# Optimization experiments

Hardware: AMD Instinct MI355X
Metric: run time of the kernel (lower is better)

The kernel has to match this reference:

```python
import jax, jax.numpy as jnp
import numpy as np

B, T, Y, H = 1024, 13, 188, 512  # batch, window, feature dim, GRU hidden
DECODE_STEPS = 13


def setup_inputs() -> dict:
    key = jax.random.key(0)
    ks = jax.random.split(key, 12)
    s = 1.0 / np.sqrt(H)  # torch GRU/Linear default init scale
    u = lambda k, shape: jax.random.uniform(k, shape, jnp.float32, -s, s)
    return {
        "x": jax.random.normal(ks[0], (B, T, Y), jnp.float32),
        # GRU layer 0 (input_size=Y)
        "W_ih0": u(ks[1], (3 * H, Y)),
        "W_hh0": u(ks[2], (3 * H, H)),
        "b_ih0": u(ks[3], (3 * H,)),
        "b_hh0": u(ks[4], (3 * H,)),
        # GRU layer 1 (input_size=H)
        "W_ih1": u(ks[5], (3 * H, H)),
        "W_hh1": u(ks[6], (3 * H, H)),
        "b_ih1": u(ks[7], (3 * H,)),
        "b_hh1": u(ks[8], (3 * H,)),
        # output Linear H -> Y
        "W_out": u(ks[9], (Y, H)),
        "b_out": u(ks[10], (Y,)),
    }


def _gru_layer(x, W_ih, W_hh, b_ih, b_hh):
    # x: [B, T, D_in]; PyTorch gate order: r, z, n. Fresh zero h0 each call.
    xg = jnp.einsum('btd,gd->btg', x, W_ih) + b_ih      # [B, T, 3H]
    xg = jnp.swapaxes(xg, 0, 1)                          # [T, B, 3H]
    h0 = jnp.zeros((x.shape[0], H), x.dtype)

    def step(h, xg_t):
        gh = h @ W_hh.T + b_hh                           # [B, 3H]
        r = jax.nn.sigmoid(xg_t[:, :H] + gh[:, :H])
        z = jax.nn.sigmoid(xg_t[:, H:2 * H] + gh[:, H:2 * H])
        n = jnp.tanh(xg_t[:, 2 * H:] + r * gh[:, 2 * H:])
        h_new = (1.0 - z) * n + z * h
        return h_new, h_new

    _, hs = jax.lax.scan(step, h0, xg)                   # [T, B, H]
    return jnp.swapaxes(hs, 0, 1)                        # [B, T, H]


def _f(x, W_ih0, W_hh0, b_ih0, b_hh0, W_ih1, W_hh1, b_ih1, b_hh1, W_out, b_out):
    h = _gru_layer(x, W_ih0, W_hh0, b_ih0, b_hh0)
    h = _gru_layer(h, W_ih1, W_hh1, b_ih1, b_hh1)
    h = jax.nn.relu(h)
    return jnp.einsum('bth,yh->bty', h, W_out) + b_out + x  # residual


def reference(x, W_ih0, W_hh0, b_ih0, b_hh0, W_ih1, W_hh1, b_ih1, b_hh1, W_out, b_out):
    params = (W_ih0, W_hh0, b_ih0, b_hh0, W_ih1, W_hh1, b_ih1, b_hh1, W_out, b_out)
    yp = []
    for _ in range(DECODE_STEPS):
        p = _f(x, *params)
        last = p[:, -1:, :]                              # [B, 1, Y]
        yp.append(last[:, 0, :])
        x = jnp.concatenate([x[:, 1:, :], last], axis=1)  # slide window
    return jnp.stack(yp, axis=1)                         # [B, 13, Y]
```

## Files before the change

kernel.cpp:

```cpp
#include <hip/hip_runtime.h>
#include <hip/hip_bf16.h>
#include <math.h>

using bf16 = __hip_bfloat16;

#define BB 1024
#define TT 13
#define YY 188
#define HH 512
#define GG 1536
#define YP 192
#define DS 13
#define NT 96
#define NTO 12

typedef __bf16 bf16x8 __attribute__((ext_vector_type(8)));
typedef float f32x4 __attribute__((ext_vector_type(4)));
typedef float f4 __attribute__((ext_vector_type(4)));

__device__ __forceinline__ float sigf(float x) { return 1.f / (1.f + expf(-x)); }
__device__ __forceinline__ bf16x8 ldf(const bf16* p) {
  return *reinterpret_cast<const bf16x8*>(p);
}
__device__ __forceinline__ f32x4 mf(bf16x8 a, bf16x8 b, f32x4 c) {
  return __builtin_amdgcn_mfma_f32_16x16x32_bf16(a, b, c, 0, 0, 0);
}
__device__ __forceinline__ void split2(float v, bf16& hi, bf16& lo) {
  hi = __float2bfloat16(v);
  lo = __float2bfloat16(v - __bfloat162float(hi));
}

struct GruPhase {
  int ncells;
  int zmask;
  unsigned a1off[13];
  unsigned hoff[13];
  unsigned ooff[13];
};

__global__ void k_swz2(const float* __restrict__ src, bf16* __restrict__ dhi,
                       bf16* __restrict__ dlo, int Nsrc, int Ksrc, int ntiles) {
  int idx = blockIdx.x * 256 + threadIdx.x;
  int l = idx & 63;
  int ktnt = idx >> 6;
  int nt = ktnt % ntiles, kt = ktnt / ntiles;
  int n = nt * 16 + (l & 15);
  int k0 = kt * 32 + (l >> 4) * 8;
#pragma unroll
  for (int j = 0; j < 8; ++j) {
    int k = k0 + j;
    float v = (n < Nsrc && k < Ksrc) ? src[(size_t)n * Ksrc + k] : 0.f;
    bf16 h, lo;
    split2(v, h, lo);
    dhi[(size_t)idx * 8 + j] = h;
    dlo[(size_t)idx * 8 + j] = lo;
  }
}

__global__ void k_setup(const float* __restrict__ x, bf16* __restrict__ th,
                        bf16* __restrict__ tl, float* __restrict__ res) {
  int idx = blockIdx.x * 256 + threadIdx.x;
  const int total = 26 * BB * YP;
  if (idx < total) {
    int k = idx % YP;
    int b = (idx / YP) % BB;
    int s = idx / (YP * BB);
    float v = 0.f;
    if (s < TT && k < YY) v = x[((size_t)b * TT + s) * YY + k];
    bf16 h, lo;
    split2(v, h, lo);
    th[idx] = h; tl[idx] = lo;
  }
  if (idx < BB * YY) {
    int yy = idx % YY;
    int b = idx / YY;
    res[idx] = x[((size_t)b * TT + 12) * YY + yy];
  }
}

template <int KT1>
__global__ __launch_bounds__(256, 2) void gru2(
    const bf16* __restrict__ a1h, const bf16* __restrict__ a1l, int lda1,
    const bf16* __restrict__ W1h, const bf16* __restrict__ W1l,
    const float* __restrict__ b1,
    const bf16* __restrict__ hbh, const bf16* __restrict__ hbl,
    const bf16* __restrict__ W2h, const bf16* __restrict__ W2l,
    const float* __restrict__ b2,
    bf16* __restrict__ obh, bf16* __restrict__ obl,
    GruPhase ph)
{
  __shared__ __align__(16) __bf16 Bl[2][24][512];
  const int tid = threadIdx.x;
  const int w = tid >> 6, l = tid & 63;
  const int lr = l & 15, lq = l >> 4, kq = lq * 8;
  const int cell = blockIdx.y >> 3, rt = blockIdx.y & 7;
  const int cw = blockIdx.x * 64;
  const int m0 = rt * 128 + w * 32;
  const bf16* A1h = a1h + ph.a1off[cell];
  const bf16* A1l = a1l + ph.a1off[cell];
  const bf16* HPh = hbh + ph.hoff[cell];
  const bf16* HPl = hbl + ph.hoff[cell];
  bf16* HOh = obh + ph.ooff[cell];
  bf16* HOl = obl + ph.ooff[cell];
  const int zero_h = (ph.zmask >> cell) & 1;
  const int KT2 = zero_h ? 0 : 16;

  const f32x4 vzero = {0.f, 0.f, 0.f, 0.f};
  f32x4 arz[2][2][4];
  f32x4 axn[2][4], ahn[2][4];
#pragma unroll
  for (int rf = 0; rf < 2; ++rf)
#pragma unroll
    for (int ntl = 0; ntl < 4; ++ntl) {
      arz[rf][0][ntl] = vzero; arz[rf][1][ntl] = vzero;
      axn[rf][ntl] = vzero; ahn[rf][ntl] = vzero;
    }

  int tl2a[6], hlr[6];
  size_t soff[6];
#pragma unroll
  for (int r = 0; r < 6; ++r) {
    const int tl2 = r * 4 + w;
    const int hl = tl2 & 1;
    const int gn = tl2 >> 1;
    const int g = gn >> 2, ntl = gn & 3;
    const int ntg = g * 32 + (cw >> 4) + ntl;
    tl2a[r] = tl2; hlr[r] = hl;
    soff[r] = ((size_t)ntg * 64 + l) * 8;
  }

  auto stage_load = [&](const bf16* Wh, const bf16* Wl2, int ktW,
                        bf16x8 (&v)[6]) {
#pragma unroll
    for (int r = 0; r < 6; ++r)
      v[r] = ldf((hlr[r] ? Wl2 : Wh) + soff[r] + (size_t)ktW * (NT * 512));
  };
  auto stage_write = [&](bf16x8 (&v)[6], int buf) {
#pragma unroll
    for (int r = 0; r < 6; ++r)
      *(bf16x8*)(&Bl[buf][tl2a[r]][l * 8]) = v[r];
  };
  auto aload = [&](const bf16* Ah, const bf16* Al, int lda, int ktA,
                   bf16x8 (&d)[2][2]) {
#pragma unroll
    for (int rf = 0; rf < 2; ++rf) {
      const size_t ao = (size_t)(m0 + rf * 16 + lr) * lda + ktA * 32 + kq;
      d[rf][0] = ldf(Ah + ao);
      d[rf][1] = ldf(Al + ao);
    }
  };
  auto compute = [&](bf16x8 (&a)[2][2], int buf, f32x4 (&an)[2][4]) {
#pragma unroll
    for (int g = 0; g < 3; ++g)
#pragma unroll
      for (int ntl = 0; ntl < 4; ++ntl) {
        int tl2 = (g * 4 + ntl) * 2;
        bf16x8 bh  = *(const bf16x8*)(&Bl[buf][tl2][l * 8]);
        bf16x8 blo = *(const bf16x8*)(&Bl[buf][tl2 + 1][l * 8]);
#pragma unroll
        for (int rf = 0; rf < 2; ++rf) {
          if (g < 2)
            arz[rf][g][ntl] = mf(a[rf][0], blo, mf(a[rf][1], bh,
                                 mf(a[rf][0], bh, arz[rf][g][ntl])));
          else
            an[rf][ntl] = mf(a[rf][0], blo, mf(a[rf][1], bh,
                             mf(a[rf][0], bh, an[rf][ntl])));
        }
      }
  };
  auto acopy = [&](bf16x8 (&dst)[2][2], bf16x8 (&src)[2][2]) {
#pragma unroll
    for (int rf = 0; rf < 2; ++rf) {
      dst[rf][0] = src[rf][0];
      dst[rf][1] = src[rf][1];
    }
  };

  bf16x8 w0[6], w1[6], acur[2][2], anx[2][2];

  stage_load(W1h, W1l, 0, w0);
  aload(A1h, A1l, lda1, 0, acur);
  stage_write(w0, 0);
  __syncthreads();

  for (int kt = 0; kt < KT1; ++kt) {
    const int buf = kt & 1;
    const bool more1 = (kt + 1 < KT1);
    const bool next = more1 || (KT2 > 0);
    if (more1)      { stage_load(W1h, W1l, kt + 1, w1); aload(A1h, A1l, lda1, kt + 1, anx); }
    else if (KT2)   { stage_load(W2h, W2l, 0, w1);      aload(HPh, HPl, HH, 0, anx); }
    compute(acur, buf, axn);
    if (next) stage_write(w1, buf ^ 1);
    __syncthreads();
    if (next) acopy(acur, anx);
  }
  if (KT2) {
    for (int kt = 0; kt < 16; ++kt) {
      const int buf = (KT1 + kt) & 1;
      const bool next = (kt + 1 < 16);
      if (next) { stage_load(W2h, W2l, kt + 1, w1); aload(HPh, HPl, HH, kt + 1, anx); }
      compute(acur, buf, ahn);
      if (next) stage_write(w1, buf ^ 1);
      __syncthreads();
      if (next) acopy(acur, anx);
    }
  }

#pragma unroll
  for (int ntl = 0; ntl < 4; ++ntl) {
    const int col = cw + ntl * 16 + lr;
    const float bx0 = b1[col], bx1 = b1[col + HH], bx2 = b1[col + 2 * HH];
    const float bh0 = b2[col], bh1 = b2[col + HH], bh2 = b2[col + 2 * HH];
#pragma unroll
    for (int rf = 0; rf < 2; ++rf)
#pragma unroll
      for (int i = 0; i < 4; ++i) {
        const int row = m0 + rf * 16 + lq * 4 + i;
        const float rr = sigf(arz[rf][0][ntl][i] + bx0 + bh0);
        const float zz = sigf(arz[rf][1][ntl][i] + bx1 + bh1);
        const float nn = tanhf(axn[rf][ntl][i] + bx2 + rr * (ahn[rf][ntl][i] + bh2));
        float hp = 0.f;
        const size_t hidx = (size_t)row * HH + col;
        if (!zero_h)
          hp = __bfloat162float(HPh[hidx]) + __bfloat162float(HPl[hidx]);
        const float hn = (1.f - zz) * nn + zz * hp;
        bf16 sh, sl;
        split2(hn, sh, sl);
        HOh[hidx] = sh;
        HOl[hidx] = sl;
      }
  }
}

template <int KT1>
__global__ __launch_bounds__(256) void gru2n(
    const bf16* __restrict__ a1h, const bf16* __restrict__ a1l, int lda1,
    const bf16* __restrict__ W1h, const bf16* __restrict__ W1l,
    const float* __restrict__ b1,
    const bf16* __restrict__ hbh, const bf16* __restrict__ hbl,
    const bf16* __restrict__ W2h, const bf16* __restrict__ W2l,
    const float* __restrict__ b2,
    bf16* __restrict__ obh, bf16* __restrict__ obl,
    GruPhase ph)
{
  __shared__ __align__(16) __bf16 Bl[2][12][512];
  const int tid = threadIdx.x;
  const int w = tid >> 6, l = tid & 63;
  const int lr = l & 15, lq = l >> 4, kq = lq * 8;
  const int cell = blockIdx.y >> 3, rt = blockIdx.y & 7;
  const int cw = blockIdx.x * 32;
  const int m0 = rt * 128 + w * 32;
  const bf16* A1h = a1h + ph.a1off[cell];
  const bf16* A1l = a1l + ph.a1off[cell];
  const bf16* HPh = hbh + ph.hoff[cell];
  const bf16* HPl = hbl + ph.hoff[cell];
  bf16* HOh = obh + ph.ooff[cell];
  bf16* HOl = obl + ph.ooff[cell];
  const int zero_h = (ph.zmask >> cell) & 1;
  const int KT2 = zero_h ? 0 : 16;

  const f32x4 vzero = {0.f, 0.f, 0.f, 0.f};
  f32x4 arz[2][2][2];
  f32x4 axn[2][2], ahn[2][2];
#pragma unroll
  for (int rf = 0; rf < 2; ++rf)
#pragma unroll
    for (int ntl = 0; ntl < 2; ++ntl) {
      arz[rf][0][ntl] = vzero; arz[rf][1][ntl] = vzero;
      axn[rf][ntl] = vzero; ahn[rf][ntl] = vzero;
    }

  int tl2a[3], uia[3], hlr[3];
  size_t soff[3];
#pragma unroll
  for (int r = 0; r < 3; ++r) {
    int u = r * 256 + tid;
    int tl2 = u >> 6;
    int ui = u & 63;
    int hl = tl2 & 1;
    int gn = tl2 >> 1;
    int g = gn >> 1, ntl = gn & 1;
    int ntg = g * 32 + (cw >> 4) + ntl;
    tl2a[r] = tl2; uia[r] = ui; hlr[r] = hl;
    soff[r] = ((size_t)ntg * 64 + ui) * 8;
  }

  auto stage_load = [&](const bf16* Wh, const bf16* Wl2, int ktW,
                        bf16x8 (&v)[3]) {
#pragma unroll
    for (int r = 0; r < 3; ++r)
      v[r] = ldf((hlr[r] ? Wl2 : Wh) + soff[r] + (size_t)ktW * (NT * 512));
  };
  auto stage_write = [&](bf16x8 (&v)[3], int buf) {
#pragma unroll
    for (int r = 0; r < 3; ++r)
      *(bf16x8*)(&Bl[buf][tl2a[r]][uia[r] * 8]) = v[r];
  };
  auto aload = [&](const bf16* Ah, const bf16* Al, int lda, int ktA,
                   bf16x8 (&d)[2][2]) {
#pragma unroll
    for (int rf = 0; rf < 2; ++rf) {
      const size_t ao = (size_t)(m0 + rf * 16 + lr) * lda + ktA * 32 + kq;
      d[rf][0] = ldf(Ah + ao);
      d[rf][1] = ldf(Al + ao);
    }
  };
  auto compute = [&](bf16x8 (&a)[2][2], int buf, f32x4 (&an)[2][2]) {
#pragma unroll
    for (int g = 0; g < 3; ++g)
#pragma unroll
      for (int ntl = 0; ntl < 2; ++ntl) {
        int tl2 = (g * 2 + ntl) * 2;
        bf16x8 bh  = *(const bf16x8*)(&Bl[buf][tl2][l * 8]);
        bf16x8 blo = *(const bf16x8*)(&Bl[buf][tl2 + 1][l * 8]);
#pragma unroll
        for (int rf = 0; rf < 2; ++rf) {
          if (g < 2)
            arz[rf][g][ntl] = mf(a[rf][0], blo, mf(a[rf][1], bh,
                                 mf(a[rf][0], bh, arz[rf][g][ntl])));
          else
            an[rf][ntl] = mf(a[rf][0], blo, mf(a[rf][1], bh,
                             mf(a[rf][0], bh, an[rf][ntl])));
        }
      }
  };
  auto acopy = [&](bf16x8 (&dst)[2][2], bf16x8 (&src)[2][2]) {
#pragma unroll
    for (int rf = 0; rf < 2; ++rf) {
      dst[rf][0] = src[rf][0];
      dst[rf][1] = src[rf][1];
    }
  };

  bf16x8 w0[3], w1[3], acur[2][2], anx[2][2];

  stage_load(W1h, W1l, 0, w0);
  aload(A1h, A1l, lda1, 0, acur);
  stage_write(w0, 0);
  __syncthreads();

  for (int kt = 0; kt < KT1; ++kt) {
    const int buf = kt & 1;
    const bool more1 = (kt + 1 < KT1);
    const bool next = more1 || (KT2 > 0);
    if (more1)      { stage_load(W1h, W1l, kt + 1, w1); aload(A1h, A1l, lda1, kt + 1, anx); }
    else if (KT2)   { stage_load(W2h, W2l, 0, w1);      aload(HPh, HPl, HH, 0, anx); }
    compute(acur, buf, axn);
    if (next) stage_write(w1, buf ^ 1);
    __syncthreads();
    if (next) acopy(acur, anx);
  }
  if (KT2) {
    for (int kt = 0; kt < 16; ++kt) {
      const int buf = (KT1 + kt) & 1;
      const bool next = (kt + 1 < 16);
      if (next) { stage_load(W2h, W2l, kt + 1, w1); aload(HPh, HPl, HH, kt + 1, anx); }
      compute(acur, buf, ahn);
      if (next) stage_write(w1, buf ^ 1);
      __syncthreads();
      if (next) acopy(acur, anx);
    }
  }

#pragma unroll
  for (int ntl = 0; ntl < 2; ++ntl) {
    const int col = cw + ntl * 16 + lr;
    const float bx0 = b1[col], bx1 = b1[col + HH], bx2 = b1[col + 2 * HH];
    const float bh0 = b2[col], bh1 = b2[col + HH], bh2 = b2[col + 2 * HH];
#pragma unroll
    for (int rf = 0; rf < 2; ++rf)
#pragma unroll
      for (int i = 0; i < 4; ++i) {
        const int row = m0 + rf * 16 + lq * 4 + i;
        const float rr = sigf(arz[rf][0][ntl][i] + bx0 + bh0);
        const float zz = sigf(arz[rf][1][ntl][i] + bx1 + bh1);
        const float nn = tanhf(axn[rf][ntl][i] + bx2 + rr * (ahn[rf][ntl][i] + bh2));
        float hp = 0.f;
        const size_t hidx = (size_t)row * HH + col;
        if (!zero_h)
          hp = __bfloat162float(HPh[hidx]) + __bfloat162float(HPl[hidx]);
        const float hn = (1.f - zz) * nn + zz * hp;
        bf16 sh, sl;
        split2(hn, sh, sl);
        HOh[hidx] = sh;
        HOl[hidx] = sl;
      }
  }
}

__global__ __launch_bounds__(256) void out_m(
    const bf16* __restrict__ h1h, const bf16* __restrict__ h1l,
    const bf16* __restrict__ Wh, const bf16* __restrict__ Wl,
    const float* __restrict__ bo,
    float* __restrict__ res,
    bf16* __restrict__ yh, bf16* __restrict__ yl,
    float* __restrict__ outp, int d)
{
  const int tid = threadIdx.x;
  const int w = tid >> 6, l = tid & 63;
  const int lr = l & 15, lq = l >> 4, kq = lq * 8;
  const int m0 = blockIdx.y * 128 + w * 32;
  const int cw = blockIdx.x * 64;

  const f32x4 vzero = {0.f, 0.f, 0.f, 0.f};
  f32x4 acc[2][4];
#pragma unroll
  for (int rf = 0; rf < 2; ++rf)
#pragma unroll
    for (int ntl = 0; ntl < 4; ++ntl) acc[rf][ntl] = vzero;

  for (int kt = 0; kt < HH / 32; ++kt) {
    bf16x8 ah[2], al[2];
#pragma unroll
    for (int rf = 0; rf < 2; ++rf) {
      const size_t ao = (size_t)(m0 + rf * 16 + lr) * HH + kt * 32 + kq;
      bf16x8 hh = ldf(h1h + ao);
      bf16x8 hl = ldf(h1l + ao);
#pragma unroll
      for (int j = 0; j < 8; ++j) {
        float v = fmaxf((float)hh[j] + (float)hl[j], 0.f);
        __bf16 vh = (__bf16)v;
        __bf16 vl = (__bf16)(v - (float)vh);
        ah[rf][j] = vh;
        al[rf][j] = vl;
      }
    }
#pragma unroll
    for (int ntl = 0; ntl < 4; ++ntl) {
      const int nt = (cw >> 4) + ntl;
      const size_t bo_ = ((size_t)(kt * NTO + nt) * 64 + l) * 8;
      bf16x8 bh = ldf(Wh + bo_);
      bf16x8 bl = ldf(Wl + bo_);
#pragma unroll
      for (int rf = 0; rf < 2; ++rf)
        acc[rf][ntl] = mf(ah[rf], bl, mf(al[rf], bh,
                          mf(ah[rf], bh, acc[rf][ntl])));
    }
  }

#pragma unroll
  for (int ntl = 0; ntl < 4; ++ntl) {
    const int col = cw + ntl * 16 + lr;
    if (col >= YY) continue;
    const float bc = bo[col];
#pragma unroll
    for (int rf = 0; rf < 2; ++rf)
#pragma unroll
      for (int i = 0; i < 4; ++i) {
        const int row = m0 + rf * 16 + lq * 4 + i;
        const int ridx = row * YY + col;
        float o = acc[rf][ntl][i] + bc + res[ridx];
        res[ridx] = o;
        outp[((size_t)row * DS + d) * YY + col] = o;
        bf16 sh, sl;
        split2(o, sh, sl);
        yh[(size_t)row * YP + col] = sh;
        yl[(size_t)row * YP + col] = sl;
      }
  }
}

extern "C" void kernel_launch(void* const* d_in, const int* in_sizes, int n_in,
                              void* d_out, int out_size, void* d_ws, size_t ws_size,
                              hipStream_t stream)
{
  static const int sig_dict[11] = {2501632, 288768, 786432, 1536, 1536,
                                   786432, 786432, 1536, 1536, 96256, 188};
  int map[11];
  bool dict_ok = (n_in == 11);
  if (dict_ok)
    for (int r = 0; r < 11; ++r)
      if (in_sizes[r] != sig_dict[r]) { dict_ok = false; break; }
  if (dict_ok) { for (int r = 0; r < 11; ++r) map[r] = r; }
  else {
    bool used[16] = {};
    for (int r = 0; r < 11; ++r) {
      map[r] = r < n_in ? r : 0;
      for (int i = 0; i < n_in && i < 16; ++i)
        if (!used[i] && in_sizes[i] == sig_dict[r]) { map[r] = i; used[i] = true; break; }
    }
  }
  const float* x     = (const float*)d_in[map[0]];
  const float* W_ih0 = (const float*)d_in[map[1]];
  const float* W_hh0 = (const float*)d_in[map[2]];
  const float* b_ih0 = (const float*)d_in[map[3]];
  const float* b_hh0 = (const float*)d_in[map[4]];
  const float* W_ih1 = (const float*)d_in[map[5]];
  const float* W_hh1 = (const float*)d_in[map[6]];
  const float* b_ih1 = (const float*)d_in[map[7]];
  const float* b_hh1 = (const float*)d_in[map[8]];
  const float* W_out = (const float*)d_in[map[9]];
  const float* b_out = (const float*)d_in[map[10]];
  float* outp = (float*)d_out;

  const int S    = (ws_size >= (size_t)160 << 20) ? 13 : 7;
  const int SKEW = (S == 13) ? 1 : 2;
  const int NPH  = 12 * SKEW + 13;

  char* p = (char*)d_ws;
  auto alloc = [&](size_t bytes) { char* q = p; p += (bytes + 255) & ~(size_t)255; return q; };
  bf16* tokh = (bf16*)alloc((size_t)26 * BB * YP * 2);
  bf16* tokl = (bf16*)alloc((size_t)26 * BB * YP * 2);
  bf16* W0h  = (bf16*)alloc((size_t)GG * YP * 2);
  bf16* W0l  = (bf16*)alloc((size_t)GG * YP * 2);
  bf16* Wh0h = (bf16*)alloc((size_t)GG * HH * 2);
  bf16* Wh0l = (bf16*)alloc((size_t)GG * HH * 2);
  bf16* Wi1h = (bf16*)alloc((size_t)GG * HH * 2);
  bf16* Wi1l = (bf16*)alloc((size_t)GG * HH * 2);
  bf16* Wh1h = (bf16*)alloc((size_t)GG * HH * 2);
  bf16* Wh1l = (bf16*)alloc((size_t)GG * HH * 2);
  bf16* Woh  = (bf16*)alloc((size_t)YP * HH * 2);
  bf16* Wol  = (bf16*)alloc((size_t)YP * HH * 2);
  bf16* h0h = (bf16*)alloc((size_t)2 * S * BB * HH * 2);
  bf16* h0l = (bf16*)alloc((size_t)2 * S * BB * HH * 2);
  bf16* h1h = (bf16*)alloc((size_t)2 * S * BB * HH * 2);
  bf16* h1l = (bf16*)alloc((size_t)2 * S * BB * HH * 2);
  float* res = (float*)alloc((size_t)BB * YY * 4);

  k_setup<<<(26 * BB * YP + 255) / 256, 256, 0, stream>>>(x, tokh, tokl, res);
  k_swz2<<<NT * (YP / 32) * 64 / 256, 256, 0, stream>>>(W_ih0, W0h, W0l, GG, YY, NT);
  k_swz2<<<NT * (HH / 32) * 64 / 256, 256, 0, stream>>>(W_hh0, Wh0h, Wh0l, GG, HH, NT);
  k_swz2<<<NT * (HH / 32) * 64 / 256, 256, 0, stream>>>(W_ih1, Wi1h, Wi1l, GG, HH, NT);
  k_swz2<<<NT * (HH / 32) * 64 / 256, 256, 0, stream>>>(W_hh1, Wh1h, Wh1l, GG, HH, NT);
  k_swz2<<<NTO * (HH / 32) * 64 / 256, 256, 0, stream>>>(W_out, Woh, Wol, YY, HH, NTO);

  for (int phs = 0; phs < NPH; ++phs) {
    GruPhase P0{}, P1{};
    const int pprev = (phs + 1) & 1, pcur = phs & 1;
    int C = 0;
    for (int d = 0; d < DS; ++d) {
      int t = phs - SKEW * d;
      if (t < 0 || t > 12) continue;
      int c = C++;
      P0.a1off[c] = (unsigned)((d + t) * BB * YP);
      P0.hoff[c]  = (unsigned)((pprev * S + d % S) * BB * HH);
      P0.ooff[c]  = (unsigned)((pcur * S + d % S) * BB * HH);
      if (t == 0) P0.zmask |= 1 << c;
      P1.a1off[c] = P0.ooff[c];
      P1.hoff[c]  = P0.hoff[c];
      P1.ooff[c]  = P0.ooff[c];
    }
    P0.ncells = P1.ncells = C;
    P1.zmask = P0.zmask;
    if (C <= 4) {
      const dim3 grid(16, C * 8);
      gru2n<YP / 32><<<grid, 256, 0, stream>>>(tokh, tokl, YP, W0h, W0l, b_ih0,
                                               h0h, h0l, Wh0h, Wh0l, b_hh0,
                                               h0h, h0l, P0);
      gru2n<HH / 32><<<grid, 256, 0, stream>>>(h0h, h0l, HH, Wi1h, Wi1l, b_ih1,
                                               h1h, h1l, Wh1h, Wh1l, b_hh1,
                                               h1h, h1l, P1);
    } else {
      const dim3 grid(8, C * 8);
      gru2<YP / 32><<<grid, 256, 0, stream>>>(tokh, tokl, YP, W0h, W0l, b_ih0,
                                              h0h, h0l, Wh0h, Wh0l, b_hh0,
                                              h0h, h0l, P0);
      gru2<HH / 32><<<grid, 256, 0, stream>>>(h0h, h0l, HH, Wi1h, Wi1l, b_ih1,
                                              h1h, h1l, Wh1h, Wh1l, b_hh1,
                                              h1h, h1l, P1);
    }
    if (phs >= 12 && (phs - 12) % SKEW == 0) {
      const int d = (phs - 12) / SKEW;
      const size_t hoff = (size_t)(pcur * S + d % S) * BB * HH;
      out_m<<<dim3(3, 8), 256, 0, stream>>>(
          h1h + hoff, h1l + hoff, Woh, Wol, b_out, res,
          tokh + (size_t)(13 + d) * BB * YP, tokl + (size_t)(13 + d) * BB * YP,
          outp, d);
    }
  }
}
```

Before: 4.207 ms.

## Swap GRU tile roles: stage activations in LDS, keep weights in registers

The large-cell GRU kernel is restructured. Each wave now owns one 16-column slice of every gate and covers all 128 rows of the block. Weight fragments for that slice are loaded straight into registers and double-buffered there, while the activation (A) tiles are staged into LDS with global_load_lds direct-to-LDS copies. This removes the register round-trip for staging and changes which operand is shared through LDS, cutting the LDS footprint from 48KB to 32KB. The accumulator count per wave stays the same but is arranged differently. Each A fragment is read 8 times per k-step from LDS, and the global_load_lds builtin's lane-to-address semantics must match the 16-byte per-lane layout.

```diff
diff --git a/kernel.cpp b/kernel.cpp
--- a/kernel.cpp
+++ b/kernel.cpp
@@ -22,12 +22,21 @@
 __device__ __forceinline__ bf16x8 ldf(const bf16* p) {
   return *reinterpret_cast<const bf16x8*>(p);
 }
+__device__ __forceinline__ bf16x8 ldf2(const void* p) {
+  return *reinterpret_cast<const bf16x8*>(p);
+}
 __device__ __forceinline__ f32x4 mf(bf16x8 a, bf16x8 b, f32x4 c) {
   return __builtin_amdgcn_mfma_f32_16x16x32_bf16(a, b, c, 0, 0, 0);
 }
 __device__ __forceinline__ void split2(float v, bf16& hi, bf16& lo) {
   hi = __float2bfloat16(v);
   lo = __float2bfloat16(v - __bfloat162float(hi));
+}
+
+typedef __attribute__((address_space(1))) const void gvoid;
+typedef __attribute__((address_space(3))) void svoid;
+__device__ __forceinline__ void glds16(const void* g, void* s) {
+  __builtin_amdgcn_global_load_lds((gvoid*)g, (svoid*)s, 16, 0, 0);
 }
 
 struct GruPhase {
@@ -79,7 +88,7 @@
 }
 
 template <int KT1>
-__global__ __launch_bounds__(256, 2) void gru2(
+__global__ __launch_bounds__(256, 2) void gru3(
     const bf16* __restrict__ a1h, const bf16* __restrict__ a1l, int lda1,
     const bf16* __restrict__ W1h, const bf16* __restrict__ W1l,
     const float* __restrict__ b1,
@@ -89,13 +98,15 @@
     bf16* __restrict__ obh, bf16* __restrict__ obl,
     GruPhase ph)
 {
-  __shared__ __align__(16) __bf16 Bl[2][24][512];
+  __shared__ __align__(16) __bf16 Als[2][16][512];
   const int tid = threadIdx.x;
   const int w = tid >> 6, l = tid & 63;
   const int lr = l & 15, lq = l >> 4, kq = lq * 8;
   const int cell = blockIdx.y >> 3, rt = blockIdx.y & 7;
   const int cw = blockIdx.x * 64;
-  const int m0 = rt * 128 + w * 32;
+  const int m0 = rt * 128;
+  const int mynt = (cw >> 4) + w;
+  const int myco = cw + w * 16;
   const bf16* A1h = a1h + ph.a1off[cell];
   const bf16* A1l = a1l + ph.a1off[cell];
   const bf16* HPh = hbh + ph.hoff[cell];
@@ -106,119 +117,93 @@
   const int KT2 = zero_h ? 0 : 16;
 
   const f32x4 vzero = {0.f, 0.f, 0.f, 0.f};
-  f32x4 arz[2][2][4];
-  f32x4 axn[2][4], ahn[2][4];
-#pragma unroll
-  for (int rf = 0; rf < 2; ++rf)
-#pragma unroll
-    for (int ntl = 0; ntl < 4; ++ntl) {
-      arz[rf][0][ntl] = vzero; arz[rf][1][ntl] = vzero;
-      axn[rf][ntl] = vzero; ahn[rf][ntl] = vzero;
-    }
-
-  int tl2a[6], hlr[6];
-  size_t soff[6];
-#pragma unroll
-  for (int r = 0; r < 6; ++r) {
-    const int tl2 = r * 4 + w;
-    const int hl = tl2 & 1;
-    const int gn = tl2 >> 1;
-    const int g = gn >> 2, ntl = gn & 3;
-    const int ntg = g * 32 + (cw >> 4) + ntl;
-    tl2a[r] = tl2; hlr[r] = hl;
-    soff[r] = ((size_t)ntg * 64 + l) * 8;
-  }
-
-  auto stage_load = [&](const bf16* Wh, const bf16* Wl2, int ktW,
-                        bf16x8 (&v)[6]) {
-#pragma unroll
-    for (int r = 0; r < 6; ++r)
-      v[r] = ldf((hlr[r] ? Wl2 : Wh) + soff[r] + (size_t)ktW * (NT * 512));
-  };
-  auto stage_write = [&](bf16x8 (&v)[6], int buf) {
-#pragma unroll
-    for (int r = 0; r < 6; ++r)
-      *(bf16x8*)(&Bl[buf][tl2a[r]][l * 8]) = v[r];
-  };
-  auto aload = [&](const bf16* Ah, const bf16* Al, int lda, int ktA,
-                   bf16x8 (&d)[2][2]) {
-#pragma unroll
-    for (int rf = 0; rf < 2; ++rf) {
-      const size_t ao = (size_t)(m0 + rf * 16 + lr) * lda + ktA * 32 + kq;
-      d[rf][0] = ldf(Ah + ao);
-      d[rf][1] = ldf(Al + ao);
-    }
-  };
-  auto compute = [&](bf16x8 (&a)[2][2], int buf, f32x4 (&an)[2][4]) {
-#pragma unroll
-    for (int g = 0; g < 3; ++g)
-#pragma unroll
-      for (int ntl = 0; ntl < 4; ++ntl) {
-        int tl2 = (g * 4 + ntl) * 2;
-        bf16x8 bh  = *(const bf16x8*)(&Bl[buf][tl2][l * 8]);
-        bf16x8 blo = *(const bf16x8*)(&Bl[buf][tl2 + 1][l * 8]);
-#pragma unroll
-        for (int rf = 0; rf < 2; ++rf) {
-          if (g < 2)
-            arz[rf][g][ntl] = mf(a[rf][0], blo, mf(a[rf][1], bh,
-                                 mf(a[rf][0], bh, arz[rf][g][ntl])));
-          else
-            an[rf][ntl] = mf(a[rf][0], blo, mf(a[rf][1], bh,
-                             mf(a[rf][0], bh, an[rf][ntl])));
-        }
+  f32x4 arz[8][2];
+  f32x4 axn[8], ahn[8];
+#pragma unroll
+  for (int rf = 0; rf < 8; ++rf) {
+    arz[rf][0] = vzero; arz[rf][1] = vzero;
+    axn[rf] = vzero; ahn[rf] = vzero;
+  }
+
+  auto stageA = [&](const bf16* Ah, const bf16* Al, int lda, int ktA, int buf) {
+#pragma unroll
+    for (int r = 0; r < 4; ++r) {
+      const int tau = w * 4 + r;
+      const int rf = tau >> 1, hl = tau & 1;
+      const bf16* src = (hl ? Al : Ah) +
+          (size_t)(m0 + rf * 16 + lr) * lda + ktA * 32 + kq;
+      glds16(src, &Als[buf][tau][0]);
+    }
+  };
+  auto wload = [&](const bf16* Wh, const bf16* Wl2, int ktW,
+                   bf16x8 (&v)[3][2]) {
+#pragma unroll
+    for (int g = 0; g < 3; ++g) {
+      const size_t o = ((size_t)(ktW * NT + g * 32 + mynt) * 64 + l) * 8;
+      v[g][0] = ldf(Wh + o);
+      v[g][1] = ldf(Wl2 + o);
+    }
+  };
+  auto compute = [&](bf16x8 (&wv)[3][2], int buf, f32x4 (&an)[8]) {
+#pragma unroll
+    for (int rf = 0; rf < 8; ++rf) {
+      bf16x8 ah = ldf2(&Als[buf][rf * 2][l * 8]);
+      bf16x8 al = ldf2(&Als[buf][rf * 2 + 1][l * 8]);
+#pragma unroll
+      for (int g = 0; g < 3; ++g) {
+        if (g < 2)
+          arz[rf][g] = mf(ah, wv[g][1], mf(al, wv[g][0],
+                          mf(ah, wv[g][0], arz[rf][g])));
+        else
+          an[rf] = mf(ah, wv[2][1], mf(al, wv[2][0],
+                      mf(ah, wv[2][0], an[rf])));
       }
-  };
-  auto acopy = [&](bf16x8 (&dst)[2][2], bf16x8 (&src)[2][2]) {
-#pragma unroll
-    for (int rf = 0; rf < 2; ++rf) {
-      dst[rf][0] = src[rf][0];
-      dst[rf][1] = src[rf][1];
-    }
-  };
-
-  bf16x8 w0[6], w1[6], acur[2][2], anx[2][2];
-
-  stage_load(W1h, W1l, 0, w0);
-  aload(A1h, A1l, lda1, 0, acur);
-  stage_write(w0, 0);
+    }
+  };
+  auto wcopy = [&](bf16x8 (&dst)[3][2], bf16x8 (&src)[3][2]) {
+#pragma unroll
+    for (int g = 0; g < 3; ++g) { dst[g][0] = src[g][0]; dst[g][1] = src[g][1]; }
+  };
+
+  bf16x8 wcur[3][2], wnext[3][2];
+
+  stageA(A1h, A1l, lda1, 0, 0);
+  wload(W1h, W1l, 0, wcur);
   __syncthreads();
 
   for (int kt = 0; kt < KT1; ++kt) {
     const int buf = kt & 1;
     const bool more1 = (kt + 1 < KT1);
-    const bool next = more1 || (KT2 > 0);
-    if (more1)      { stage_load(W1h, W1l, kt + 1, w1); aload(A1h, A1l, lda1, kt + 1, anx); }
-    else if (KT2)   { stage_load(W2h, W2l, 0, w1);      aload(HPh, HPl, HH, 0, anx); }
-    compute(acur, buf, axn);
-    if (next) stage_write(w1, buf ^ 1);
+    const bool next = more1 || (KT2 != 0);
+    if (more1)     { stageA(A1h, A1l, lda1, kt + 1, buf ^ 1); wload(W1h, W1l, kt + 1, wnext); }
+    else if (KT2)  { stageA(HPh, HPl, HH, 0, buf ^ 1);        wload(W2h, W2l, 0, wnext); }
+    compute(wcur, buf, axn);
     __syncthreads();
-    if (next) acopy(acur, anx);
+    if (next) wcopy(wcur, wnext);
   }
   if (KT2) {
     for (int kt = 0; kt < 16; ++kt) {
       const int buf = (KT1 + kt) & 1;
       const bool next = (kt + 1 < 16);
-      if (next) { stage_load(W2h, W2l, kt + 1, w1); aload(HPh, HPl, HH, kt + 1, anx); }
-      compute(acur, buf, ahn);
-      if (next) stage_write(w1, buf ^ 1);
+      if (next) { stageA(HPh, HPl, HH, kt + 1, buf ^ 1); wload(W2h, W2l, kt + 1, wnext); }
+      compute(wcur, buf, ahn);
       __syncthreads();
-      if (next) acopy(acur, anx);
-    }
-  }
-
-#pragma unroll
-  for (int ntl = 0; ntl < 4; ++ntl) {
-    const int col = cw + ntl * 16 + lr;
+      if (next) wcopy(wcur, wnext);
+    }
+  }
+
+  {
+    const int col = myco + lr;
     const float bx0 = b1[col], bx1 = b1[col + HH], bx2 = b1[col + 2 * HH];
     const float bh0 = b2[col], bh1 = b2[col + HH], bh2 = b2[col + 2 * HH];
 #pragma unroll
-    for (int rf = 0; rf < 2; ++rf)
+    for (int rf = 0; rf < 8; ++rf)
 #pragma unroll
       for (int i = 0; i < 4; ++i) {
         const int row = m0 + rf * 16 + lq * 4 + i;
-        const float rr = sigf(arz[rf][0][ntl][i] + bx0 + bh0);
-        const float zz = sigf(arz[rf][1][ntl][i] + bx1 + bh1);
-        const float nn = tanhf(axn[rf][ntl][i] + bx2 + rr * (ahn[rf][ntl][i] + bh2));
+        const float rr = sigf(arz[rf][0][i] + bx0 + bh0);
+        const float zz = sigf(arz[rf][1][i] + bx1 + bh1);
+        const float nn = tanhf(axn[rf][i] + bx2 + rr * (ahn[rf][i] + bh2));
         float hp = 0.f;
         const size_t hidx = (size_t)row * HH + col;
         if (!zero_h)
@@ -552,10 +537,10 @@
                                                h1h, h1l, P1);
     } else {
       const dim3 grid(8, C * 8);
-      gru2<YP / 32><<<grid, 256, 0, stream>>>(tokh, tokl, YP, W0h, W0l, b_ih0,
+      gru3<YP / 32><<<grid, 256, 0, stream>>>(tokh, tokl, YP, W0h, W0l, b_ih0,
                                               h0h, h0l, Wh0h, Wh0l, b_hh0,
                                               h0h, h0l, P0);
-      gru2<HH / 32><<<grid, 256, 0, stream>>>(h0h, h0l, HH, Wi1h, Wi1l, b_ih1,
+      gru3<HH / 32><<<grid, 256, 0, stream>>>(h0h, h0l, HH, Wi1h, Wi1l, b_ih1,
                                               h1h, h1l, Wh1h, Wh1l, b_hh1,
                                               h1h, h1l, P1);
     }
```

Result: slower. 4.465 ms (+6.1%).
